# Optimization experiments

Hardware: AMD Instinct MI355X
Metric: run time of the kernel (lower is better)

Reference implementation:

```python
import jax, jax.numpy as jnp
import numpy as np

B, N, F = 64, 128, 4
H = 100


def setup_inputs() -> dict:
    key = jax.random.key(0)
    ks = jax.random.split(key, 8)
    x = jax.random.normal(ks[0], (B, N, F), dtype=jnp.float32)
    in_hitnr = jax.random.randint(ks[1], (B, N), 0, N, dtype=jnp.int32)
    W1 = jax.random.normal(ks[2], (2 * F, H), dtype=jnp.float32) * (1.0 / np.sqrt(2 * F))
    b1 = jax.random.normal(ks[3], (H,), dtype=jnp.float32) * 0.01
    W2 = jax.random.normal(ks[4], (H, H), dtype=jnp.float32) * (1.0 / np.sqrt(H))
    b2 = jax.random.normal(ks[5], (H,), dtype=jnp.float32) * 0.01
    W3 = jax.random.normal(ks[6], (H, 1), dtype=jnp.float32) * (1.0 / np.sqrt(H))
    b3 = jax.random.normal(ks[7], (1,), dtype=jnp.float32) * 0.01
    return {"x": x, "in_hitnr": in_hitnr, "W1": W1, "b1": b1,
            "W2": W2, "b2": b2, "W3": W3, "b3": b3}


def reference(x, in_hitnr, W1, b1, W2, b2, W3, b3):
    n = x.shape[1]
    # itertools.combinations(range(n), 2) == lexicographic upper-triangle order
    i1, i2 = jnp.triu_indices(n, k=1)  # each [num_pairs]
    # pairwise gather + concat: [B, P, 2F]
    pairs = jnp.concatenate([x[:, i1], x[:, i2]], axis=-1)
    h = pairs @ W1 + b1                 # [B, P, 100]
    h = h @ W2 + b2                     # [B, P, 100]
    h = jax.nn.relu(h)                  # ReLU applied AFTER second linear (as in source)
    out = h @ W3 + b3                   # [B, P, 1]
    out = jax.nn.sigmoid(out)
    return jnp.squeeze(out, axis=-1)    # [B, P]
```

## Files before the change

### kernel.cpp

```cpp
#include <hip/hip_runtime.h>
#include <math.h>


namespace {
constexpr int B_    = 64;
constexpr int N_    = 128;
constexpr int H_    = 100;
constexpr int TILE  = 16;
constexpr int NT    = N_ / TILE;
constexpr int NTP   = NT * (NT + 1) / 2;
constexpr int PAIRS = N_ * (N_ - 1) / 2;
constexpr int FOLD_AB = 0;
constexpr int FOLD_C  = 800;
constexpr int FOLD_W3 = 900;
constexpr int FOLD_B3 = 1000;
}

__device__ float g_fold[1001];

__global__ __launch_bounds__(256)
void fold_weights(const float* __restrict__ W1, const float* __restrict__ b1,
                  const float* __restrict__ W2, const float* __restrict__ b2,
                  const float* __restrict__ W3, const float* __restrict__ b3)
{
    const int idx = blockIdx.x * 256 + threadIdx.x;
    if (idx < 800) {
        const int r = idx / H_;
        const int h = idx - r * H_;
        const float* w1r = W1 + r * H_;
        float s = 0.f;
        #pragma unroll 5
        for (int j = 0; j < H_; ++j) s = fmaf(w1r[j], W2[j * H_ + h], s);
        g_fold[FOLD_AB + idx] = s;
    } else if (idx < 900) {
        const int h = idx - 800;
        float s = b2[h];
        #pragma unroll 5
        for (int j = 0; j < H_; ++j) s = fmaf(b1[j], W2[j * H_ + h], s);
        g_fold[FOLD_C + h] = s;
    } else if (idx < 1000) {
        g_fold[FOLD_W3 + (idx - 900)] = W3[idx - 900];
    } else if (idx == 1000) {
        g_fold[FOLD_B3] = b3[0];
    }
}

__global__ __launch_bounds__(64)
void pairnet_main(const float* __restrict__ x, float* __restrict__ out)
{
    __shared__ float U_s[50 * 2 * TILE];
    __shared__ float V_s[50 * 2 * TILE];
    __shared__ float w3_s[H_];

    const int tid = threadIdx.x;
    const int blk = blockIdx.x;
    const int b   = blk / NTP;
    int rem = blk - b * NTP;
    int ti = 0;
    while (rem >= NT - ti) { rem -= NT - ti; ++ti; }
    const int tj = ti + rem;
    const int i0 = ti * TILE, j0 = tj * TILE;

    for (int k = tid; k < H_; k += 64) w3_s[k] = g_fold[FOLD_W3 + k];

    const float4* x4 = (const float4*)x;
    for (int idx = tid; idx < TILE * H_; idx += 64) {
        const int r = idx & (TILE - 1);
        const int h = idx >> 4;
        const int a = (h >> 1) * (2 * TILE) + r * 2 + (h & 1);
        const float4 xi = x4[b * N_ + i0 + r];
        U_s[a] = g_fold[FOLD_C + h]
               + xi.x * g_fold[FOLD_AB + 0 * H_ + h]
               + xi.y * g_fold[FOLD_AB + 1 * H_ + h]
               + xi.z * g_fold[FOLD_AB + 2 * H_ + h]
               + xi.w * g_fold[FOLD_AB + 3 * H_ + h];
        const float4 xj = x4[b * N_ + j0 + r];
        V_s[a] = xj.x * g_fold[FOLD_AB + 4 * H_ + h]
               + xj.y * g_fold[FOLD_AB + 5 * H_ + h]
               + xj.z * g_fold[FOLD_AB + 6 * H_ + h]
               + xj.w * g_fold[FOLD_AB + 7 * H_ + h];
    }
    __syncthreads();

    const int i2 = tid >> 3;
    const int j2 = tid & 7;
    const int ia = 2 * i2, ja = 2 * j2;
    float a00 = 0.f, a01 = 0.f, a10 = 0.f, a11 = 0.f;
    #pragma unroll 2
    for (int h2 = 0; h2 < 50; ++h2) {
        const float2 w = *(const float2*)&w3_s[2 * h2];
        const float4 u = *(const float4*)&U_s[h2 * 32 + ia * 2];
        const float4 v = *(const float4*)&V_s[h2 * 32 + ja * 2];
        a00 = fmaf(w.x, fmaxf(u.x + v.x, 0.f), fmaf(w.y, fmaxf(u.y + v.y, 0.f), a00));
        a01 = fmaf(w.x, fmaxf(u.x + v.z, 0.f), fmaf(w.y, fmaxf(u.y + v.w, 0.f), a01));
        a10 = fmaf(w.x, fmaxf(u.z + v.x, 0.f), fmaf(w.y, fmaxf(u.w + v.y, 0.f), a10));
        a11 = fmaf(w.x, fmaxf(u.z + v.z, 0.f), fmaf(w.y, fmaxf(u.w + v.w, 0.f), a11));
    }

    const float b3v = g_fold[FOLD_B3];
    float* outb = out + b * PAIRS;
    const float accs[2][2] = {{a00, a01}, {a10, a11}};
    #pragma unroll
    for (int da = 0; da < 2; ++da) {
        #pragma unroll
        for (int dc = 0; dc < 2; ++dc) {
            const int gi = i0 + ia + da;
            const int gj = j0 + ja + dc;
            if (gi < gj) {
                const int p = (gi * (2 * N_ - gi - 1)) / 2 + (gj - gi - 1);
                const float z = accs[da][dc] + b3v;
                outb[p] = 1.f / (1.f + __expf(-z));
            }
        }
    }
}

extern "C" void kernel_launch(void* const* d_in, const int* in_sizes, int n_in,
                              void* d_out, int out_size, void* d_ws, size_t ws_size,
                              hipStream_t stream) {
    const float* x  = (const float*)d_in[0];
    const float* W1 = (const float*)d_in[2];
    const float* b1 = (const float*)d_in[3];
    const float* W2 = (const float*)d_in[4];
    const float* b2 = (const float*)d_in[5];
    const float* W3 = (const float*)d_in[6];
    const float* b3 = (const float*)d_in[7];
    float* out = (float*)d_out;

    fold_weights<<<dim3(4), dim3(256), 0, stream>>>(W1, b1, W2, b2, W3, b3);
    pairnet_main<<<dim3(B_ * NTP), dim3(64), 0, stream>>>(x, out);
}
```

Before: 89.23 us.

## Precompute U/V projections in separate kernel and enlarge pair tiles

Splits the per-point projection (U and V) into its own kernel that writes to workspace, so each pair block loads precomputed values instead of recomputing them per tile. Pair tiles grow from 16 to 32 with 128 threads, each computing a 4x2 micro-tile over the full hidden dimension. This cuts redundant projection arithmetic and improves register reuse, but adds a kernel launch and a global round-trip for U/V, and leaves fewer, larger blocks.

After: 99.83 us. 1.12x slower.

```diff
diff --git a/kernel.cpp b/kernel.cpp
--- a/kernel.cpp
+++ b/kernel.cpp
@@ -6,7 +6,7 @@
 constexpr int B_    = 64;
 constexpr int N_    = 128;
 constexpr int H_    = 100;
-constexpr int TILE  = 16;
+constexpr int TILE  = 32;
 constexpr int NT    = N_ / TILE;
 constexpr int NTP   = NT * (NT + 1) / 2;
 constexpr int PAIRS = N_ * (N_ - 1) / 2;
@@ -14,6 +14,7 @@
 constexpr int FOLD_C  = 800;
 constexpr int FOLD_W3 = 900;
 constexpr int FOLD_B3 = 1000;
+constexpr int UVSZ    = B_ * H_ * N_;
 }
 
 __device__ float g_fold[1001];
@@ -45,14 +46,39 @@
     }
 }
 
-__global__ __launch_bounds__(64)
-void pairnet_main(const float* __restrict__ x, float* __restrict__ out)
+__global__ __launch_bounds__(256)
+void compute_uv(const float* __restrict__ x,
+                float* __restrict__ Uw, float* __restrict__ Vw)
 {
-    __shared__ float U_s[50 * 2 * TILE];
-    __shared__ float V_s[50 * 2 * TILE];
-    __shared__ float w3_s[H_];
+    const int t   = threadIdx.x;
+    const int blk = blockIdx.x;
+    const int b   = blk / 50;
+    const int h   = (blk - b * 50) * 2 + (t >> 7);
+    const int n   = t & 127;
+    const float4 xv = ((const float4*)x)[b * N_ + n];
+    const float u = g_fold[FOLD_C + h]
+        + xv.x * g_fold[FOLD_AB + 0 * H_ + h]
+        + xv.y * g_fold[FOLD_AB + 1 * H_ + h]
+        + xv.z * g_fold[FOLD_AB + 2 * H_ + h]
+        + xv.w * g_fold[FOLD_AB + 3 * H_ + h];
+    const float v =
+          xv.x * g_fold[FOLD_AB + 4 * H_ + h]
+        + xv.y * g_fold[FOLD_AB + 5 * H_ + h]
+        + xv.z * g_fold[FOLD_AB + 6 * H_ + h]
+        + xv.w * g_fold[FOLD_AB + 7 * H_ + h];
+    const int o = (b * H_ + h) * N_ + n;
+    Uw[o] = u;
+    Vw[o] = v;
+}
 
-    const int tid = threadIdx.x;
+__global__ __launch_bounds__(128)
+void pairnet_pair(const float* __restrict__ Uw, const float* __restrict__ Vw,
+                  float* __restrict__ out)
+{
+    __shared__ float U_s[H_][TILE];
+    __shared__ float V_s[H_][TILE];
+
+    const int t   = threadIdx.x;
     const int blk = blockIdx.x;
     const int b   = blk / NTP;
     int rem = blk - b * NTP;
@@ -61,55 +87,46 @@
     const int tj = ti + rem;
     const int i0 = ti * TILE, j0 = tj * TILE;
 
-    for (int k = tid; k < H_; k += 64) w3_s[k] = g_fold[FOLD_W3 + k];
-
-    const float4* x4 = (const float4*)x;
-    for (int idx = tid; idx < TILE * H_; idx += 64) {
-        const int r = idx & (TILE - 1);
-        const int h = idx >> 4;
-        const int a = (h >> 1) * (2 * TILE) + r * 2 + (h & 1);
-        const float4 xi = x4[b * N_ + i0 + r];
-        U_s[a] = g_fold[FOLD_C + h]
-               + xi.x * g_fold[FOLD_AB + 0 * H_ + h]
-               + xi.y * g_fold[FOLD_AB + 1 * H_ + h]
-               + xi.z * g_fold[FOLD_AB + 2 * H_ + h]
-               + xi.w * g_fold[FOLD_AB + 3 * H_ + h];
-        const float4 xj = x4[b * N_ + j0 + r];
-        V_s[a] = xj.x * g_fold[FOLD_AB + 4 * H_ + h]
-               + xj.y * g_fold[FOLD_AB + 5 * H_ + h]
-               + xj.z * g_fold[FOLD_AB + 6 * H_ + h]
-               + xj.w * g_fold[FOLD_AB + 7 * H_ + h];
+    const float4* U4 = (const float4*)Uw;
+    const float4* V4 = (const float4*)Vw;
+    for (int idx = t; idx < 800; idx += 128) {
+        const int h = idx >> 3, q = idx & 7;
+        *(float4*)&U_s[h][4 * q] = U4[(b * H_ + h) * 32 + 8 * ti + q];
+    }
+    for (int idx = t; idx < 800; idx += 128) {
+        const int h = idx >> 3, q = idx & 7;
+        *(float4*)&V_s[h][4 * q] = V4[(b * H_ + h) * 32 + 8 * tj + q];
     }
     __syncthreads();
 
-    const int i2 = tid >> 3;
-    const int j2 = tid & 7;
-    const int ia = 2 * i2, ja = 2 * j2;
-    float a00 = 0.f, a01 = 0.f, a10 = 0.f, a11 = 0.f;
+    const int iq = t >> 4;
+    const int jq = t & 15;
+    float acc[4][2] = {};
     #pragma unroll 2
-    for (int h2 = 0; h2 < 50; ++h2) {
-        const float2 w = *(const float2*)&w3_s[2 * h2];
-        const float4 u = *(const float4*)&U_s[h2 * 32 + ia * 2];
-        const float4 v = *(const float4*)&V_s[h2 * 32 + ja * 2];
-        a00 = fmaf(w.x, fmaxf(u.x + v.x, 0.f), fmaf(w.y, fmaxf(u.y + v.y, 0.f), a00));
-        a01 = fmaf(w.x, fmaxf(u.x + v.z, 0.f), fmaf(w.y, fmaxf(u.y + v.w, 0.f), a01));
-        a10 = fmaf(w.x, fmaxf(u.z + v.x, 0.f), fmaf(w.y, fmaxf(u.w + v.y, 0.f), a10));
-        a11 = fmaf(w.x, fmaxf(u.z + v.z, 0.f), fmaf(w.y, fmaxf(u.w + v.w, 0.f), a11));
+    for (int h = 0; h < H_; ++h) {
+        const float  w = g_fold[FOLD_W3 + h];
+        const float4 u = *(const float4*)&U_s[h][4 * iq];
+        const float2 v = *(const float2*)&V_s[h][2 * jq];
+        const float us[4] = {u.x, u.y, u.z, u.w};
+        const float vs[2] = {v.x, v.y};
+        #pragma unroll
+        for (int r = 0; r < 4; ++r)
+            #pragma unroll
+            for (int c = 0; c < 2; ++c)
+                acc[r][c] = fmaf(w, fmaxf(us[r] + vs[c], 0.f), acc[r][c]);
     }
 
     const float b3v = g_fold[FOLD_B3];
     float* outb = out + b * PAIRS;
-    const float accs[2][2] = {{a00, a01}, {a10, a11}};
     #pragma unroll
-    for (int da = 0; da < 2; ++da) {
+    for (int r = 0; r < 4; ++r) {
         #pragma unroll
-        for (int dc = 0; dc < 2; ++dc) {
-            const int gi = i0 + ia + da;
-            const int gj = j0 + ja + dc;
+        for (int c = 0; c < 2; ++c) {
+            const int gi = i0 + 4 * iq + r;
+            const int gj = j0 + 2 * jq + c;
             if (gi < gj) {
                 const int p = (gi * (2 * N_ - gi - 1)) / 2 + (gj - gi - 1);
-                const float z = accs[da][dc] + b3v;
-                outb[p] = 1.f / (1.f + __expf(-z));
+                outb[p] = 1.f / (1.f + __expf(-(acc[r][c] + b3v)));
             }
         }
     }
@@ -127,6 +144,10 @@
     const float* b3 = (const float*)d_in[7];
     float* out = (float*)d_out;
 
-    fold_weights<<<dim3(4), dim3(256), 0, stream>>>(W1, b1, W2, b2, W3, b3);
-    pairnet_main<<<dim3(B_ * NTP), dim3(64), 0, stream>>>(x, out);
+    float* Uw = (float*)d_ws;
+    float* Vw = Uw + UVSZ;
+
+    fold_weights<<<dim3(4),        dim3(256), 0, stream>>>(W1, b1, W2, b2, W3, b3);
+    compute_uv  <<<dim3(B_ * 50),  dim3(256), 0, stream>>>(x, Uw, Vw);
+    pairnet_pair<<<dim3(B_ * NTP), dim3(128), 0, stream>>>(Uw, Vw, out);
 }
```

## Enlarge pair tiles to 32, stage folded weights in shared memory with row-major layout

Applied to the files above, without the earlier changes.

Tile size grows from 16 to 32 and blocks go from 64 to 256 threads, so each block covers four times as many pairs and there are fewer blocks with fewer wasted lower-triangle tiles. The folded weights are stored per hidden unit in padded rows of 12, copied into shared memory with vector loads, and the U/V projections are built from vectorized shared reads. This cuts the scattered global reads of the fold table and the per-block overhead, at the cost of more shared memory per block and fewer blocks overall.

After: 85.62 us. -4.1%, faster.

```diff
diff --git a/kernel.cpp b/kernel.cpp
--- a/kernel.cpp
+++ b/kernel.cpp
@@ -6,53 +6,53 @@
 constexpr int B_    = 64;
 constexpr int N_    = 128;
 constexpr int H_    = 100;
-constexpr int TILE  = 16;
+constexpr int TILE  = 32;
 constexpr int NT    = N_ / TILE;
 constexpr int NTP   = NT * (NT + 1) / 2;
 constexpr int PAIRS = N_ * (N_ - 1) / 2;
-constexpr int FOLD_AB = 0;
-constexpr int FOLD_C  = 800;
-constexpr int FOLD_W3 = 900;
-constexpr int FOLD_B3 = 1000;
+constexpr int FROW  = 12;
+constexpr int FW3   = H_ * FROW;
+constexpr int FB3   = FW3 + H_;
+constexpr int FTOT  = 1304;
 }
 
-__device__ float g_fold[1001];
+__device__ __align__(16) float g_fold2[FTOT];
 
-__global__ __launch_bounds__(256)
+__global__ __launch_bounds__(128)
 void fold_weights(const float* __restrict__ W1, const float* __restrict__ b1,
                   const float* __restrict__ W2, const float* __restrict__ b2,
                   const float* __restrict__ W3, const float* __restrict__ b3)
 {
-    const int idx = blockIdx.x * 256 + threadIdx.x;
+    const int idx = blockIdx.x * 128 + threadIdx.x;
     if (idx < 800) {
-        const int r = idx / H_;
-        const int h = idx - r * H_;
-        const float* w1r = W1 + r * H_;
+        const int k = idx / H_;
+        const int h = idx - k * H_;
+        const float* w1r = W1 + k * H_;
         float s = 0.f;
         #pragma unroll 5
         for (int j = 0; j < H_; ++j) s = fmaf(w1r[j], W2[j * H_ + h], s);
-        g_fold[FOLD_AB + idx] = s;
+        g_fold2[h * FROW + k] = s;
     } else if (idx < 900) {
         const int h = idx - 800;
         float s = b2[h];
         #pragma unroll 5
         for (int j = 0; j < H_; ++j) s = fmaf(b1[j], W2[j * H_ + h], s);
-        g_fold[FOLD_C + h] = s;
+        g_fold2[h * FROW + 8] = s;
     } else if (idx < 1000) {
-        g_fold[FOLD_W3 + (idx - 900)] = W3[idx - 900];
+        g_fold2[FW3 + (idx - 900)] = W3[idx - 900];
     } else if (idx == 1000) {
-        g_fold[FOLD_B3] = b3[0];
+        g_fold2[FB3] = b3[0];
     }
 }
 
-__global__ __launch_bounds__(64)
-void pairnet_main(const float* __restrict__ x, float* __restrict__ out)
+__global__ __launch_bounds__(256)
+void pairnet(const float* __restrict__ x, float* __restrict__ out)
 {
-    __shared__ float U_s[50 * 2 * TILE];
-    __shared__ float V_s[50 * 2 * TILE];
-    __shared__ float w3_s[H_];
+    __shared__ __align__(16) float fold_s[FTOT];
+    __shared__ __align__(16) float U_s[50 * TILE * 2];
+    __shared__ __align__(16) float V_s[50 * TILE * 2];
 
-    const int tid = threadIdx.x;
+    const int t   = threadIdx.x;
     const int blk = blockIdx.x;
     const int b   = blk / NTP;
     int rem = blk - b * NTP;
@@ -61,43 +61,54 @@
     const int tj = ti + rem;
     const int i0 = ti * TILE, j0 = tj * TILE;
 
-    for (int k = tid; k < H_; k += 64) w3_s[k] = g_fold[FOLD_W3 + k];
+    {
+        const float4* gf4 = (const float4*)g_fold2;
+        float4* fs4 = (float4*)fold_s;
+        fs4[t & 255] = gf4[t & 255];
+        if (t < FTOT / 4 - 256) fs4[256 + t] = gf4[256 + t];
+    }
+    const int r = t & 31;
+    const float4 xi = ((const float4*)x)[b * N_ + i0 + r];
+    const float4 xj = ((const float4*)x)[b * N_ + j0 + r];
+    __syncthreads();
 
-    const float4* x4 = (const float4*)x;
-    for (int idx = tid; idx < TILE * H_; idx += 64) {
-        const int r = idx & (TILE - 1);
-        const int h = idx >> 4;
-        const int a = (h >> 1) * (2 * TILE) + r * 2 + (h & 1);
-        const float4 xi = x4[b * N_ + i0 + r];
-        U_s[a] = g_fold[FOLD_C + h]
-               + xi.x * g_fold[FOLD_AB + 0 * H_ + h]
-               + xi.y * g_fold[FOLD_AB + 1 * H_ + h]
-               + xi.z * g_fold[FOLD_AB + 2 * H_ + h]
-               + xi.w * g_fold[FOLD_AB + 3 * H_ + h];
-        const float4 xj = x4[b * N_ + j0 + r];
-        V_s[a] = xj.x * g_fold[FOLD_AB + 4 * H_ + h]
-               + xj.y * g_fold[FOLD_AB + 5 * H_ + h]
-               + xj.z * g_fold[FOLD_AB + 6 * H_ + h]
-               + xj.w * g_fold[FOLD_AB + 7 * H_ + h];
+    for (int k = 0; k < 7; ++k) {
+        const int idx = t + k * 256;
+        if (idx < 1600) {
+            const int h2 = idx >> 5;
+            const float* row0 = &fold_s[(2 * h2) * FROW];
+            const float* row1 = &fold_s[(2 * h2 + 1) * FROW];
+            const float4 a0 = *(const float4*)(row0);
+            const float4 b0 = *(const float4*)(row0 + 4);
+            const float4 a1 = *(const float4*)(row1);
+            const float4 b1v = *(const float4*)(row1 + 4);
+            float2 u, v;
+            u.x = row0[8] + xi.x*a0.x + xi.y*a0.y + xi.z*a0.z + xi.w*a0.w;
+            u.y = row1[8] + xi.x*a1.x + xi.y*a1.y + xi.z*a1.z + xi.w*a1.w;
+            v.x =           xj.x*b0.x + xj.y*b0.y + xj.z*b0.z + xj.w*b0.w;
+            v.y =           xj.x*b1v.x + xj.y*b1v.y + xj.z*b1v.z + xj.w*b1v.w;
+            *(float2*)&U_s[h2 * 64 + r * 2] = u;
+            *(float2*)&V_s[h2 * 64 + r * 2] = v;
+        }
     }
     __syncthreads();
 
-    const int i2 = tid >> 3;
-    const int j2 = tid & 7;
-    const int ia = 2 * i2, ja = 2 * j2;
+    const int iq = t >> 4;
+    const int jq = t & 15;
+    const int ia = 2 * iq, ja = 2 * jq;
     float a00 = 0.f, a01 = 0.f, a10 = 0.f, a11 = 0.f;
     #pragma unroll 2
     for (int h2 = 0; h2 < 50; ++h2) {
-        const float2 w = *(const float2*)&w3_s[2 * h2];
-        const float4 u = *(const float4*)&U_s[h2 * 32 + ia * 2];
-        const float4 v = *(const float4*)&V_s[h2 * 32 + ja * 2];
+        const float2 w = *(const float2*)&fold_s[FW3 + 2 * h2];
+        const float4 u = *(const float4*)&U_s[h2 * 64 + ia * 2];
+        const float4 v = *(const float4*)&V_s[h2 * 64 + ja * 2];
         a00 = fmaf(w.x, fmaxf(u.x + v.x, 0.f), fmaf(w.y, fmaxf(u.y + v.y, 0.f), a00));
         a01 = fmaf(w.x, fmaxf(u.x + v.z, 0.f), fmaf(w.y, fmaxf(u.y + v.w, 0.f), a01));
         a10 = fmaf(w.x, fmaxf(u.z + v.x, 0.f), fmaf(w.y, fmaxf(u.w + v.y, 0.f), a10));
         a11 = fmaf(w.x, fmaxf(u.z + v.z, 0.f), fmaf(w.y, fmaxf(u.w + v.w, 0.f), a11));
     }
 
-    const float b3v = g_fold[FOLD_B3];
+    const float b3v = fold_s[FB3];
     float* outb = out + b * PAIRS;
     const float accs[2][2] = {{a00, a01}, {a10, a11}};
     #pragma unroll
@@ -108,8 +119,7 @@
             const int gj = j0 + ja + dc;
             if (gi < gj) {
                 const int p = (gi * (2 * N_ - gi - 1)) / 2 + (gj - gi - 1);
-                const float z = accs[da][dc] + b3v;
-                outb[p] = 1.f / (1.f + __expf(-z));
+                outb[p] = 1.f / (1.f + __expf(-(accs[da][dc] + b3v)));
             }
         }
     }
@@ -127,6 +137,6 @@
     const float* b3 = (const float*)d_in[7];
     float* out = (float*)d_out;
 
-    fold_weights<<<dim3(4), dim3(256), 0, stream>>>(W1, b1, W2, b2, W3, b3);
-    pairnet_main<<<dim3(B_ * NTP), dim3(64), 0, stream>>>(x, out);
+    fold_weights<<<dim3(8),        dim3(128), 0, stream>>>(W1, b1, W2, b2, W3, b3);
+    pairnet     <<<dim3(B_ * NTP), dim3(256), 0, stream>>>(x, out);
 }
```
